# Kernel tuning notes

Hardware: AMD Instinct MI355X
Metric: run time of the kernel (lower is better)

## Reference

```python
import jax, jax.numpy as jnp
import numpy as np
import math

B, S, E, H, L, C, DFF = 8, 1024, 512, 8, 2, 8921, 2048
DH = E // H
LN_EPS = 1e-5


def _make_pe(max_len, d):
    pos = np.arange(max_len, dtype=np.float32)[:, None]
    div = np.exp(np.arange(0, d, 2, dtype=np.float32) * (-math.log(10000.0) / d))
    pe = np.zeros((max_len, d), dtype=np.float32)
    pe[:, 0::2] = np.sin(pos * div)
    pe[:, 1::2] = np.cos(pos * div)
    return jnp.asarray(pe)


def setup_inputs() -> dict:
    key = jax.random.key(0)
    ks = jax.random.split(key, 16)
    sc = 0.02
    return {
        'inputs': jax.random.normal(ks[0], (B, S, E), jnp.float32),
        'pe': _make_pe(S, E),
        'label_mat': jax.random.normal(ks[1], (C, E), jnp.float32) * sc,
        'l1_w': jax.random.normal(ks[2], (E, E), jnp.float32) * sc,
        'l1_b': jnp.zeros((E,), jnp.float32),
        'fc_w': jax.random.normal(ks[3], (C, E), jnp.float32) * sc,
        'fc_b': jnp.zeros((C,), jnp.float32),
        'in_proj_w': jax.random.normal(ks[4], (L, 3 * E, E), jnp.float32) * sc,
        'in_proj_b': jnp.zeros((L, 3 * E), jnp.float32),
        'out_proj_w': jax.random.normal(ks[5], (L, E, E), jnp.float32) * sc,
        'out_proj_b': jnp.zeros((L, E), jnp.float32),
        'ln1_w': jnp.ones((L, E), jnp.float32),
        'ln1_b': jnp.zeros((L, E), jnp.float32),
        'ln2_w': jnp.ones((L, E), jnp.float32),
        'ln2_b': jnp.zeros((L, E), jnp.float32),
        'lin1_w': jax.random.normal(ks[6], (L, DFF, E), jnp.float32) * sc,
        'lin1_b': jnp.zeros((L, DFF), jnp.float32),
        'lin2_w': jax.random.normal(ks[7], (L, E, DFF), jnp.float32) * sc,
        'lin2_b': jnp.zeros((L, E), jnp.float32),
    }


def _ln(x, g, b):
    mu = jnp.mean(x, axis=-1, keepdims=True)
    v = jnp.mean(jnp.square(x - mu), axis=-1, keepdims=True)
    return (x - mu) * jax.lax.rsqrt(v + LN_EPS) * g + b


def _encoder_layer(x, wqkv, bqkv, wo, bo, g1, b1, g2, b2, w1, bb1, w2, bb2):
    # x: [B,S,E]; post-norm torch TransformerEncoderLayer with relu
    qkv = x @ wqkv.T + bqkv                      # [B,S,3E]
    q, k, v = jnp.split(qkv, 3, axis=-1)
    q = q.reshape(B, S, H, DH)
    k = k.reshape(B, S, H, DH)
    v = v.reshape(B, S, H, DH)
    scores = jnp.einsum('bqhd,bkhd->bhqk', q, k) / math.sqrt(DH)
    attn = jax.nn.softmax(scores, axis=-1)
    o = jnp.einsum('bhqk,bkhd->bqhd', attn, v).reshape(B, S, E)
    o = o @ wo.T + bo
    x = _ln(x + o, g1, b1)
    ff = jax.nn.relu(x @ w1.T + bb1) @ w2.T + bb2
    return _ln(x + ff, g2, b2)


def reference(inputs, pe, label_mat, l1_w, l1_b, fc_w, fc_b,
              in_proj_w, in_proj_b, out_proj_w, out_proj_b,
              ln1_w, ln1_b, ln2_w, ln2_b,
              lin1_w, lin1_b, lin2_w, lin2_b):
    # faithful to source: pe is indexed by batch position (source bug)
    x = inputs * math.sqrt(E) + pe[:B][:, None, :]      # [B,S,E]
    for i in range(L):
        x = _encoder_layer(x, in_proj_w[i], in_proj_b[i], out_proj_w[i], out_proj_b[i],
                           ln1_w[i], ln1_b[i], ln2_w[i], ln2_b[i],
                           lin1_w[i], lin1_b[i], lin2_w[i], lin2_b[i])
    # label attention
    o1 = jnp.tanh(x @ l1_w.T + l1_b)                    # [B,S,E]
    scores = o1 @ label_mat.T                           # [B,S,C]
    attn_weights = jax.nn.softmax(scores, axis=1)       # over seq dim
    attn_weights = jnp.swapaxes(attn_weights, 1, 2)     # [B,C,S]
    weighted = attn_weights @ x                         # [B,C,E]
    # fused per-class linears: C tiny GEMVs -> one einsum
    outputs = jnp.einsum('bce,ce->bc', weighted, fc_w) + fc_b  # [B,C]
    return outputs, attn_weights
```

## Files before the change

kernel.cpp:

```cpp
#include <hip/hip_runtime.h>
#include <math.h>

#define BB   8
#define SS   1024
#define EE   512
#define HH   8
#define DHH  64
#define LLY  2
#define CC   8921
#define CP   9088
#define DFF_ 2048

typedef short          bf16x8 __attribute__((ext_vector_type(8)));
typedef float          f32x4  __attribute__((ext_vector_type(4)));
typedef unsigned short u16x4  __attribute__((ext_vector_type(4)));
typedef unsigned short u16x8  __attribute__((ext_vector_type(8)));

__device__ __forceinline__ float bf2f(unsigned short u) {
    return __uint_as_float(((unsigned int)u) << 16);
}
__device__ __forceinline__ unsigned short f2bf(float f) {
    unsigned int u = __float_as_uint(f);
    u = (u + 0x7FFFu + ((u >> 16) & 1u)) >> 16;
    return (unsigned short)u;
}
__device__ __forceinline__ void gload16(const void* g, void* l) {
    __builtin_amdgcn_global_load_lds(
        (const __attribute__((address_space(1))) void*)g,
        (__attribute__((address_space(3))) void*)l, 16, 0, 0);
}

__global__ __launch_bounds__(256) void cvt_bf16(const float* __restrict__ in,
                                                unsigned short* __restrict__ out,
                                                long n_in, long n_out)
{
    const long i4 = ((long)blockIdx.x * 256 + threadIdx.x) * 4;
    if (i4 >= n_out) return;
    u16x4 r;
    if (i4 < n_in) {
        const float4 v = *(const float4*)(in + i4);
        r[0] = f2bf(v.x); r[1] = f2bf(v.y); r[2] = f2bf(v.z); r[3] = f2bf(v.w);
    } else {
        r[0] = r[1] = r[2] = r[3] = 0;
    }
    *(u16x4*)(out + i4) = r;
}

__global__ __launch_bounds__(256) void embed_kernel(const float* __restrict__ in,
                                                    const float* __restrict__ pe,
                                                    float* __restrict__ x,
                                                    unsigned short* __restrict__ xb)
{
    const long i  = (long)blockIdx.x * 256 + threadIdx.x;
    const int  e4 = (int)(i & 127);
    const int  b  = (int)(i >> 17);
    float4 v = ((const float4*)in)[i];
    const float4 p = ((const float4*)pe)[b * 128 + e4];
    const float sc = 22.627416997969522f;
    v.x = v.x * sc + p.x;  v.y = v.y * sc + p.y;
    v.z = v.z * sc + p.z;  v.w = v.w * sc + p.w;
    ((float4*)x)[i] = v;
    u16x4 h; h[0] = f2bf(v.x); h[1] = f2bf(v.y); h[2] = f2bf(v.z); h[3] = f2bf(v.w);
    ((u16x4*)xb)[i] = h;
}

template<int FN>
__global__ __launch_bounds__(256) void gemm_mfma_t(const unsigned short* __restrict__ A,
                                                   const unsigned short* __restrict__ B,
                                                   const float* __restrict__ bias,
                                                   float* __restrict__ Cf,
                                                   unsigned short* __restrict__ Ch,
                                                   int M, int N, int K, int Mlim,
                                                   long sAz, long sBz, long sCz,
                                                   int act, int mode)
{
    __shared__ unsigned short As[128 * 64];
    __shared__ unsigned short Bs[32 * FN * 64];
    const int t  = threadIdx.x;
    const int wv = t >> 6, ln = t & 63;
    const int wr = wv >> 1, wc = wv & 1;
    const int lr = ln & 15, lg = ln >> 4;
    const int m0 = blockIdx.x * 128, n0 = blockIdx.y * (32 * FN);
    const int z  = blockIdx.z;
    const unsigned short* Ab = A + (long)z * sAz;
    const unsigned short* Bb = B + (long)z * sBz;

    const int srow = ln >> 3;
    const int ucol = ((ln & 7) ^ srow) << 3;

    f32x4 acc[4][FN];
    #pragma unroll
    for (int i = 0; i < 4; ++i)
        #pragma unroll
        for (int j = 0; j < FN; ++j)
            acc[i][j] = (f32x4){0.f, 0.f, 0.f, 0.f};

    int rA[4], rB[FN];
    #pragma unroll
    for (int f = 0; f < 4; ++f) rA[f] = wr * 64 + f * 16 + lr;
    #pragma unroll
    for (int f = 0; f < FN; ++f) rB[f] = wc * (16 * FN) + f * 16 + lr;

    for (int k0 = 0; k0 < K; k0 += 64) {
        __syncthreads();
        #pragma unroll
        for (int c = 0; c < 4; ++c) {
            const int q   = (wv << 2) + c;
            const int row = (q << 3) + srow;
            gload16(Ab + (long)(m0 + row) * K + k0 + ucol, (char*)As + (q << 10));
        }
        #pragma unroll
        for (int c = 0; c < FN; ++c) {
            const int q   = wv * FN + c;
            const int row = (q << 3) + srow;
            gload16(Bb + (long)(n0 + row) * K + k0 + ucol, (char*)Bs + (q << 10));
        }
        __syncthreads();
        #pragma unroll
        for (int kk = 0; kk < 2; ++kk) {
            bf16x8 af[4], bg[FN];
            const int s = (kk << 2) + lg;
            #pragma unroll
            for (int f = 0; f < 4; ++f)
                af[f] = *(const bf16x8*)((const char*)As + rA[f] * 128 + ((s ^ (rA[f] & 7)) << 4));
            #pragma unroll
            for (int f = 0; f < FN; ++f)
                bg[f] = *(const bf16x8*)((const char*)Bs + rB[f] * 128 + ((s ^ (rB[f] & 7)) << 4));
            #pragma unroll
            for (int i = 0; i < 4; ++i)
                #pragma unroll
                for (int j = 0; j < FN; ++j)
                    acc[i][j] = __builtin_amdgcn_mfma_f32_16x16x32_bf16(af[i], bg[j], acc[i][j], 0, 0, 0);
        }
    }

    const long zC = (long)z * sCz;
    #pragma unroll
    for (int fm = 0; fm < 4; ++fm) {
        #pragma unroll
        for (int reg = 0; reg < 4; ++reg) {
            const int gm = m0 + wr * 64 + fm * 16 + lg * 4 + reg;
            if (gm >= Mlim) continue;
            #pragma unroll
            for (int fn = 0; fn < FN; ++fn) {
                const int gn = n0 + wc * (16 * FN) + fn * 16 + lr;
                float v = acc[fm][fn][reg];
                if (bias) v += bias[gn];
                if (act == 1)      v = fmaxf(v, 0.f);
                else if (act == 2) v = tanhf(v);
                if (mode & 1) Cf[zC + (long)gm * N + gn] = v;
                if (mode & 2) Ch[zC + (long)gm * N + gn] = f2bf(v);
            }
        }
    }
}

__device__ __forceinline__ void label_swizzle(int& bx, int& by, int& bz)
{
    const int flat = blockIdx.x + 71 * (blockIdx.y + 8 * blockIdx.z);
    const int swz  = (flat & 7) * 568 + (flat >> 3);
    bx = swz >> 6;
    by = swz & 7;
    bz = (swz >> 3) & 7;
}

template<bool BF16RAW>
__global__ __launch_bounds__(256) void gemm_scores_t(const unsigned short* __restrict__ A,
                                                     const unsigned short* __restrict__ B,
                                                     float* __restrict__ attnW,
                                                     unsigned short* __restrict__ rawb,
                                                     float2* __restrict__ stats)
{
    __shared__ unsigned short As[128 * 64];
    __shared__ unsigned short Bs[128 * 64];
    int bx, by, bz;
    label_swizzle(bx, by, bz);
    const int t  = threadIdx.x;
    const int wv = t >> 6, ln = t & 63;
    const int wr = wv >> 1, wc = wv & 1;
    const int lr = ln & 15, lg = ln >> 4;
    const int m0 = bx * 128, n0 = by * 128;
    const int z  = bz;
    const unsigned short* Bb = B + (long)z * SS * EE;

    const int srow = ln >> 3;
    const int ucol = ((ln & 7) ^ srow) << 3;

    f32x4 acc[4][4];
    #pragma unroll
    for (int i = 0; i < 4; ++i)
        #pragma unroll
        for (int j = 0; j < 4; ++j)
            acc[i][j] = (f32x4){0.f, 0.f, 0.f, 0.f};

    int rA[4], rB[4];
    #pragma unroll
    for (int f = 0; f < 4; ++f) {
        rA[f] = wr * 64 + f * 16 + lr;
        rB[f] = wc * 64 + f * 16 + lr;
    }

    for (int k0 = 0; k0 < EE; k0 += 64) {
        __syncthreads();
        #pragma unroll
        for (int c = 0; c < 4; ++c) {
            const int q   = (wv << 2) + c;
            const int row = (q << 3) + srow;
            gload16(A  + (long)(m0 + row) * EE + k0 + ucol, (char*)As + (q << 10));
            gload16(Bb + (long)(n0 + row) * EE + k0 + ucol, (char*)Bs + (q << 10));
        }
        __syncthreads();
        #pragma unroll
        for (int kk = 0; kk < 2; ++kk) {
            bf16x8 af[4], bg[4];
            const int s = (kk << 2) + lg;
            #pragma unroll
            for (int f = 0; f < 4; ++f) {
                af[f] = *(const bf16x8*)((const char*)As + rA[f] * 128 + ((s ^ (rA[f] & 7)) << 4));
                bg[f] = *(const bf16x8*)((const char*)Bs + rB[f] * 128 + ((s ^ (rB[f] & 7)) << 4));
            }
            #pragma unroll
            for (int i = 0; i < 4; ++i)
                #pragma unroll
                for (int j = 0; j < 4; ++j)
                    acc[i][j] = __builtin_amdgcn_mfma_f32_16x16x32_bf16(af[i], bg[j], acc[i][j], 0, 0, 0);
        }
    }

    float* aw = attnW + (long)z * CC * SS;
    unsigned short* rb = rawb + (long)z * CC * SS;
    #pragma unroll
    for (int fm = 0; fm < 4; ++fm) {
        #pragma unroll
        for (int reg = 0; reg < 4; ++reg) {
            const int r = m0 + wr * 64 + fm * 16 + lg * 4 + reg;
            const float v0 = acc[fm][0][reg], v1 = acc[fm][1][reg];
            const float v2 = acc[fm][2][reg], v3 = acc[fm][3][reg];
            if (r < CC) {
                #pragma unroll
                for (int fn = 0; fn < 4; ++fn) {
                    const int sn = n0 + wc * 64 + fn * 16 + lr;
                    if (BF16RAW) rb[(long)r * SS + sn] = f2bf(acc[fm][fn][reg]);
                    else         aw[(long)r * SS + sn] = acc[fm][fn][reg];
                }
            }
            float mx = fmaxf(fmaxf(v0, v1), fmaxf(v2, v3));
            mx = fmaxf(mx, __shfl_xor(mx, 1));
            mx = fmaxf(mx, __shfl_xor(mx, 2));
            mx = fmaxf(mx, __shfl_xor(mx, 4));
            mx = fmaxf(mx, __shfl_xor(mx, 8));
            float sm = __expf(v0 - mx) + __expf(v1 - mx) + __expf(v2 - mx) + __expf(v3 - mx);
            sm += __shfl_xor(sm, 1); sm += __shfl_xor(sm, 2);
            sm += __shfl_xor(sm, 4); sm += __shfl_xor(sm, 8);
            if (lr == 0 && r < CC)
                stats[((long)z * CP + r) * 16 + by * 2 + wc] = make_float2(mx, sm);
        }
    }
}

__global__ __launch_bounds__(256) void merge_stats(const float2* __restrict__ stats,
                                                   float2* __restrict__ rowstat)
{
    const long idx = (long)blockIdx.x * 256 + threadIdx.x;
    if (idx >= (long)BB * CP) return;
    const int c = (int)(idx % CP);
    if (c >= CC) return;
    const float2* s = stats + idx * 16;
    float mx = -1e30f;
    #pragma unroll
    for (int i = 0; i < 16; ++i) mx = fmaxf(mx, s[i].x);
    float tot = 0.f;
    #pragma unroll
    for (int i = 0; i < 16; ++i) tot += s[i].y * __expf(s[i].x - mx);
    rowstat[idx] = make_float2(mx, 1.f / tot);
}

template<bool BF16RAW>
__global__ __launch_bounds__(256) void gemm_label_final_t(const unsigned short* __restrict__ A,
                                                          const unsigned short* __restrict__ B,
                                                          float* __restrict__ attnW,
                                                          const unsigned short* __restrict__ rawb,
                                                          const float2* __restrict__ rowstat,
                                                          float* __restrict__ out)
{
    __shared__ unsigned short As[128 * 64];
    __shared__ unsigned short Bs[128 * 64];
    int bx, by, bz;
    label_swizzle(bx, by, bz);
    const int t  = threadIdx.x;
    const int wv = t >> 6, ln = t & 63;
    const int wr = wv >> 1, wc = wv & 1;
    const int lr = ln & 15, lg = ln >> 4;
    const int m0 = bx * 128, n0 = by * 128;
    const int z  = bz;
    const unsigned short* Bb = B + (long)z * SS * EE;

    const int srow = ln >> 3;
    const int ucol = ((ln & 7) ^ srow) << 3;

    f32x4 acc[4][4];
    #pragma unroll
    for (int i = 0; i < 4; ++i)
        #pragma unroll
        for (int j = 0; j < 4; ++j)
            acc[i][j] = (f32x4){0.f, 0.f, 0.f, 0.f};

    int rA[4], rB[4];
    #pragma unroll
    for (int f = 0; f < 4; ++f) {
        rA[f] = wr * 64 + f * 16 + lr;
        rB[f] = wc * 64 + f * 16 + lr;
    }

    for (int k0 = 0; k0 < EE; k0 += 64) {
        __syncthreads();
        #pragma unroll
        for (int c = 0; c < 4; ++c) {
            const int q   = (wv << 2) + c;
            const int row = (q << 3) + srow;
            gload16(A  + (long)(m0 + row) * EE + k0 + ucol, (char*)As + (q << 10));
            gload16(Bb + (long)(n0 + row) * EE + k0 + ucol, (char*)Bs + (q << 10));
        }
        __syncthreads();
        #pragma unroll
        for (int kk = 0; kk < 2; ++kk) {
            bf16x8 af[4], bg[4];
            const int s = (kk << 2) + lg;
            #pragma unroll
            for (int f = 0; f < 4; ++f) {
                af[f] = *(const bf16x8*)((const char*)As + rA[f] * 128 + ((s ^ (rA[f] & 7)) << 4));
                bg[f] = *(const bf16x8*)((const char*)Bs + rB[f] * 128 + ((s ^ (rB[f] & 7)) << 4));
            }
            #pragma unroll
            for (int i = 0; i < 4; ++i)
                #pragma unroll
                for (int j = 0; j < 4; ++j)
                    acc[i][j] = __builtin_amdgcn_mfma_f32_16x16x32_bf16(af[i], bg[j], acc[i][j], 0, 0, 0);
        }
    }

    float* aw = attnW + (long)z * CC * SS;
    const unsigned short* rb = rawb + (long)z * CC * SS;
    const float2* rs = rowstat + (long)z * CP;
    float* outb = out + (long)z * CC;
    #pragma unroll
    for (int fm = 0; fm < 4; ++fm) {
        #pragma unroll
        for (int reg = 0; reg < 4; ++reg) {
            const int r = m0 + wr * 64 + fm * 16 + lg * 4 + reg;
            float pacc = 0.f;
            if (r < CC) {
                const float2 st = rs[r];
                #pragma unroll
                for (int fn = 0; fn < 4; ++fn) {
                    const int sn = n0 + wc * 64 + fn * 16 + lr;
                    const float raw = BF16RAW ? bf2f(rb[(long)r * SS + sn])
                                              : aw[(long)r * SS + sn];
                    const float p = __expf(raw - st.x) * st.y;
                    aw[(long)r * SS + sn] = p;
                    pacc += p * acc[fm][fn][reg];
                }
            }
            pacc += __shfl_xor(pacc, 1);
            pacc += __shfl_xor(pacc, 2);
            pacc += __shfl_xor(pacc, 4);
            pacc += __shfl_xor(pacc, 8);
            if (lr == 0 && r < CC) atomicAdd(&outb[r], pacc);
        }
    }
}

__global__ __launch_bounds__(256) void vtrans(const unsigned short* __restrict__ qkv,
                                              unsigned short* __restrict__ Vt)
{
    __shared__ unsigned short tile[64][72];
    const int bh = blockIdx.y, b = bh >> 3, h = bh & 7;
    const int s0 = blockIdx.x << 6;
    const int t  = threadIdx.x;
    const int r  = t >> 3;
    const int c8 = (t & 7) << 3;
    const unsigned short* vb = qkv + (long)b * SS * 1536 + 2 * EE + h * DHH;
    #pragma unroll
    for (int rr = 0; rr < 64; rr += 32)
        *(u16x8*)&tile[r + rr][c8] = *(const u16x8*)(vb + (long)(s0 + r + rr) * 1536 + c8);
    __syncthreads();
    #pragma unroll
    for (int rr = 0; rr < 64; rr += 32) {
        const int d = r + rr;
        u16x8 o;
        #pragma unroll
        for (int j = 0; j < 8; ++j) o[j] = tile[c8 + j][d];
        *(u16x8*)(Vt + ((long)bh * DHH + d) * SS + s0 + c8) = o;
    }
}

__global__ __launch_bounds__(512) void flash_mfma(const unsigned short* __restrict__ qkv,
                                                  const unsigned short* __restrict__ Vt,
                                                  unsigned short* __restrict__ o)
{
    __shared__ unsigned short sK[64 * 64];
    __shared__ unsigned short sV[64 * 64];
    __shared__ unsigned short sP[8][16 * 64];
    const int t  = threadIdx.x;
    const int wv = t >> 6, ln = t & 63;
    const int lr = ln & 15, lg = ln >> 4;
    const int bh = blockIdx.y, b = bh >> 3, h = bh & 7;
    const int q0 = (blockIdx.x << 7) + (wv << 4);

    const unsigned short* qb = qkv + (long)b * SS * 1536 + h * DHH;
    const unsigned short* kb = qb + EE;
    const unsigned short* vt = Vt + (long)bh * DHH * SS;
    unsigned short* pw = sP[wv];

    const int srow = ln >> 3;
    const int ucol = ((ln & 7) ^ srow) << 3;

    bf16x8 aq[2];
    #pragma unroll
    for (int c = 0; c < 2; ++c)
        aq[c] = *(const bf16x8*)(qb + (long)(q0 + lr) * 1536 + (c << 5) + (lg << 3));

    float m_[4], l_[4];
    f32x4 accO[4];
    #pragma unroll
    for (int r = 0; r < 4; ++r) { m_[r] = -1e30f; l_[r] = 0.f; }
    #pragma unroll
    for (int n = 0; n < 4; ++n) accO[n] = (f32x4){0.f, 0.f, 0.f, 0.f};

    for (int s0 = 0; s0 < SS; s0 += 64) {
        __syncthreads();
        {
            const int row = (wv << 3) + srow;
            gload16(kb + (long)(s0 + row) * 1536 + ucol, (char*)sK + (wv << 10));
            gload16(vt + (long)row * SS + s0 + ucol,     (char*)sV + (wv << 10));
        }
        __syncthreads();

        f32x4 accS[4];
        #pragma unroll
        for (int sj = 0; sj < 4; ++sj) accS[sj] = (f32x4){0.f, 0.f, 0.f, 0.f};
        #pragma unroll
        for (int c = 0; c < 2; ++c) {
            const int slot = (c << 2) + lg;
            #pragma unroll
            for (int sj = 0; sj < 4; ++sj) {
                const int rw = (sj << 4) + lr;
                const bf16x8 kf = *(const bf16x8*)((const char*)sK + rw * 128 + ((slot ^ (rw & 7)) << 4));
                accS[sj] = __builtin_amdgcn_mfma_f32_16x16x32_bf16(aq[c], kf, accS[sj], 0, 0, 0);
            }
        }
        #pragma unroll
        for (int reg = 0; reg < 4; ++reg) {
            float sc0 = accS[0][reg] * 0.125f, sc1 = accS[1][reg] * 0.125f;
            float sc2 = accS[2][reg] * 0.125f, sc3 = accS[3][reg] * 0.125f;
            float mx = fmaxf(fmaxf(sc0, sc1), fmaxf(sc2, sc3));
            mx = fmaxf(mx, __shfl_xor(mx, 1));
            mx = fmaxf(mx, __shfl_xor(mx, 2));
            mx = fmaxf(mx, __shfl_xor(mx, 4));
            mx = fmaxf(mx, __shfl_xor(mx, 8));
            const float mnew = fmaxf(m_[reg], mx);
            const float f = __expf(m_[reg] - mnew);
            m_[reg] = mnew;
            sc0 = __expf(sc0 - mnew); sc1 = __expf(sc1 - mnew);
            sc2 = __expf(sc2 - mnew); sc3 = __expf(sc3 - mnew);
            accS[0][reg] = sc0; accS[1][reg] = sc1;
            accS[2][reg] = sc2; accS[3][reg] = sc3;
            float ss = sc0 + sc1 + sc2 + sc3;
            ss += __shfl_xor(ss, 1); ss += __shfl_xor(ss, 2);
            ss += __shfl_xor(ss, 4); ss += __shfl_xor(ss, 8);
            l_[reg] = l_[reg] * f + ss;
            #pragma unroll
            for (int n = 0; n < 4; ++n) accO[n][reg] *= f;
        }
        #pragma unroll
        for (int sj = 0; sj < 4; ++sj) {
            #pragma unroll
            for (int reg = 0; reg < 4; ++reg) {
                const int q = (lg << 2) + reg;
                const int s = (sj << 4) + lr;
                const int byte = (q << 7) + (((s >> 3) ^ (q & 7)) << 4) + ((s & 7) << 1);
                *(unsigned short*)((char*)pw + byte) = f2bf(accS[sj][reg]);
            }
        }
        #pragma unroll
        for (int c2 = 0; c2 < 2; ++c2) {
            const int pslot = ((c2 << 2) + lg) ^ (lr & 7);
            const bf16x8 pa = *(const bf16x8*)((const char*)pw + (lr << 7) + (pslot << 4));
            const int vslot = (c2 << 2) + lg;
            #pragma unroll
            for (int n = 0; n < 4; ++n) {
                const int rw = (n << 4) + lr;
                const bf16x8 vf = *(const bf16x8*)((const char*)sV + rw * 128 + ((vslot ^ (rw & 7)) << 4));
                accO[n] = __builtin_amdgcn_mfma_f32_16x16x32_bf16(pa, vf, accO[n], 0, 0, 0);
            }
        }
    }

    #pragma unroll
    for (int reg = 0; reg < 4; ++reg) {
        const float inv = 1.f / l_[reg];
        unsigned short* orow = o + (long)(b * SS + q0 + (lg << 2) + reg) * EE + h * DHH;
        #pragma unroll
        for (int n = 0; n < 4; ++n)
            orow[(n << 4) + lr] = f2bf(accO[n][reg] * inv);
    }
}

__global__ __launch_bounds__(256) void ln_fused(float* __restrict__ x,
                                                unsigned short* __restrict__ xb,
                                                const float* __restrict__ o,
                                                const float* __restrict__ g,
                                                const float* __restrict__ bta)
{
    const long row = blockIdx.x;
    float* xr = x + row * EE;
    unsigned short* hb = xb + row * EE;
    const float* orr = o + row * EE;
    const int t = threadIdx.x;
    const float v0 = xr[t] + orr[t];
    const float v1 = xr[t + 256] + orr[t + 256];
    float s = v0 + v1;
    #pragma unroll
    for (int off = 1; off < 64; off <<= 1) s += __shfl_xor(s, off);
    __shared__ float r1[4], r2[4];
    if ((t & 63) == 0) r1[t >> 6] = s;
    __syncthreads();
    const float mu = (r1[0] + r1[1] + r1[2] + r1[3]) * (1.f / EE);
    const float d0 = v0 - mu, d1 = v1 - mu;
    float q = d0 * d0 + d1 * d1;
    #pragma unroll
    for (int off = 1; off < 64; off <<= 1) q += __shfl_xor(q, off);
    if ((t & 63) == 0) r2[t >> 6] = q;
    __syncthreads();
    const float rs = rsqrtf((r2[0] + r2[1] + r2[2] + r2[3]) * (1.f / EE) + 1e-5f);
    const float y0 = d0 * rs * g[t]       + bta[t];
    const float y1 = d1 * rs * g[t + 256] + bta[t + 256];
    xr[t] = y0;  xr[t + 256] = y1;
    hb[t] = f2bf(y0);  hb[t + 256] = f2bf(y1);
}

__global__ __launch_bounds__(256) void init_out(float* __restrict__ out,
                                                const float* __restrict__ fcb)
{
    const int i = blockIdx.x * 256 + threadIdx.x;
    if (i < BB * CC) out[i] = fcb[i % CC];
}

extern "C" void kernel_launch(void* const* d_in, const int* in_sizes, int n_in,
                              void* d_out, int out_size, void* d_ws, size_t ws_size,
                              hipStream_t stream)
{
    const float* inp   = (const float*)d_in[0];
    const float* pe    = (const float*)d_in[1];
    const float* label = (const float*)d_in[2];
    const float* l1w   = (const float*)d_in[3];
    const float* l1b   = (const float*)d_in[4];
    const float* fcw   = (const float*)d_in[5];
    const float* fcb   = (const float*)d_in[6];
    const float* ipw   = (const float*)d_in[7];
    const float* ipb   = (const float*)d_in[8];
    const float* opw   = (const float*)d_in[9];
    const float* opb   = (const float*)d_in[10];
    const float* g1    = (const float*)d_in[11];
    const float* b1    = (const float*)d_in[12];
    const float* g2    = (const float*)d_in[13];
    const float* b2    = (const float*)d_in[14];
    const float* w1    = (const float*)d_in[15];
    const float* bb1   = (const float*)d_in[16];
    const float* w2    = (const float*)d_in[17];
    const float* bb2   = (const float*)d_in[18];

    char* wp = (char*)d_ws;
    float* x = (float*)wp;                 wp += (long)BB * SS * EE * 4;
    unsigned short* xb = (unsigned short*)wp;  wp += (long)BB * SS * EE * 2;
    float* bufo = (float*)wp;              wp += (long)BB * SS * EE * 4;
    unsigned short* big = (unsigned short*)wp; wp += (long)BB * SS * DFF_ * 2;
    unsigned short* ob  = (unsigned short*)wp; wp += (long)BB * SS * EE * 2;
    unsigned short* Vtb = (unsigned short*)wp; wp += (long)BB * HH * DHH * SS * 2;
    unsigned short* ipwb = (unsigned short*)wp; wp += (long)LLY * 3 * EE * EE * 2;
    unsigned short* opwb = (unsigned short*)wp; wp += (long)LLY * EE * EE * 2;
    unsigned short* w1b  = (unsigned short*)wp; wp += (long)LLY * DFF_ * EE * 2;
    unsigned short* w2b  = (unsigned short*)wp; wp += (long)LLY * EE * DFF_ * 2;
    unsigned short* l1wb = (unsigned short*)wp; wp += (long)EE * EE * 2;
    unsigned short* labelb = (unsigned short*)wp; wp += (long)CP * EE * 2;
    unsigned short* fcwb   = (unsigned short*)wp; wp += (long)CP * EE * 2;
    float2* stats   = (float2*)wp;         wp += (long)BB * CP * 16 * 8;
    float2* rowstat = (float2*)wp;         wp += (long)BB * CP * 8;
    unsigned short* rawb = (unsigned short*)wp;
    const long raw_bytes = (long)BB * CC * SS * 2;
    const bool bf16raw = ((long)ws_size >= (wp - (char*)d_ws) + raw_bytes);

    float* out0  = (float*)d_out;
    float* attnW = out0 + BB * CC;

    {
        const long n1 = (long)LLY * 3 * EE * EE;
        cvt_bf16<<<(int)((n1 / 4 + 255) / 256), 256, 0, stream>>>(ipw, ipwb, n1, n1);
        const long n2 = (long)LLY * EE * EE;
        cvt_bf16<<<(int)((n2 / 4 + 255) / 256), 256, 0, stream>>>(opw, opwb, n2, n2);
        const long n3 = (long)LLY * DFF_ * EE;
        cvt_bf16<<<(int)((n3 / 4 + 255) / 256), 256, 0, stream>>>(w1, w1b, n3, n3);
        cvt_bf16<<<(int)((n3 / 4 + 255) / 256), 256, 0, stream>>>(w2, w2b, n3, n3);
        const long n4 = (long)EE * EE;
        cvt_bf16<<<(int)((n4 / 4 + 255) / 256), 256, 0, stream>>>(l1w, l1wb, n4, n4);
        const long n5i = (long)CC * EE, n5o = (long)CP * EE;
        cvt_bf16<<<(int)((n5o / 4 + 255) / 256), 256, 0, stream>>>(label, labelb, n5i, n5o);
        cvt_bf16<<<(int)((n5o / 4 + 255) / 256), 256, 0, stream>>>(fcw, fcwb, n5i, n5o);
    }

    const int M = BB * SS;

    embed_kernel<<<4096, 256, 0, stream>>>(inp, pe, x, xb);

    for (int l = 0; l < LLY; ++l) {
        gemm_mfma_t<4><<<dim3(64, 12, 1), 256, 0, stream>>>(xb, ipwb + (long)l * 3 * EE * EE,
                                                            ipb + l * 3 * EE, nullptr, big,
                                                            M, 3 * EE, EE, M, 0, 0, 0, 0, 2);
        vtrans<<<dim3(16, 64), 256, 0, stream>>>(big, Vtb);
        flash_mfma<<<dim3(8, 64), 512, 0, stream>>>(big, Vtb, ob);
        gemm_mfma_t<2><<<dim3(64, 8, 1), 256, 0, stream>>>(ob, opwb + (long)l * EE * EE,
                                                           opb + l * EE, bufo, nullptr,
                                                           M, EE, EE, M, 0, 0, 0, 0, 1);
        ln_fused<<<M, 256, 0, stream>>>(x, xb, bufo, g1 + l * EE, b1 + l * EE);
        gemm_mfma_t<4><<<dim3(64, 16, 1), 256, 0, stream>>>(xb, w1b + (long)l * DFF_ * EE,
                                                            bb1 + l * DFF_, nullptr, big,
                                                            M, DFF_, EE, M, 0, 0, 0, 1, 2);
        gemm_mfma_t<2><<<dim3(64, 8, 1), 256, 0, stream>>>(big, w2b + (long)l * EE * DFF_,
                                                           bb2 + l * EE, bufo, nullptr,
                                                           M, EE, DFF_, M, 0, 0, 0, 0, 1);
        ln_fused<<<M, 256, 0, stream>>>(x, xb, bufo, g2 + l * EE, b2 + l * EE);
    }

    gemm_mfma_t<2><<<dim3(64, 8, 1), 256, 0, stream>>>(xb, l1wb, l1b, nullptr, ob,
                                                       M, EE, EE, M, 0, 0, 0, 2, 2);
    if (bf16raw)
        gemm_scores_t<true><<<dim3(CP / 128, SS / 128, BB), 256, 0, stream>>>(labelb, ob, attnW, rawb, stats);
    else
        gemm_scores_t<false><<<dim3(CP / 128, SS / 128, BB), 256, 0, stream>>>(labelb, ob, attnW, rawb, stats);
    merge_stats<<<(int)(((long)BB * CP + 255) / 256), 256, 0, stream>>>(stats, rowstat);
    init_out<<<(BB * CC + 255) / 256, 256, 0, stream>>>(out0, fcb);
    if (bf16raw)
        gemm_label_final_t<true><<<dim3(CP / 128, SS / 128, BB), 256, 0, stream>>>(fcwb, xb, attnW, rawb, rowstat, out0);
    else
        gemm_label_final_t<false><<<dim3(CP / 128, SS / 128, BB), 256, 0, stream>>>(fcwb, xb, attnW, rawb, rowstat, out0);
}
```

Measured before the change: 1.012 ms.

## Loop over sequence tiles inside label-final GEMM to cut atomics

The final label GEMM kernel now launches one block per (class tile, batch) and loops over all eight sequence tiles internally. Per-row partial sums accumulate in registers, so each class row gets one atomicAdd instead of eight. The cost is 8x fewer blocks (568 instead of 4544), which lowers parallelism and latency hiding on a large GPU, and the block swizzle is replaced with a simple custom mapping.

```diff
diff --git a/kernel.cpp b/kernel.cpp
--- a/kernel.cpp
+++ b/kernel.cpp
@@ -275,6 +275,13 @@
     rowstat[idx] = make_float2(mx, 1.f / tot);
 }
 
+__global__ __launch_bounds__(256) void init_out(float* __restrict__ out,
+                                                const float* __restrict__ fcb)
+{
+    const int i = blockIdx.x * 256 + threadIdx.x;
+    if (i < BB * CC) out[i] = fcb[i % CC];
+}
+
 template<bool BF16RAW>
 __global__ __launch_bounds__(256) void gemm_label_final_t(const unsigned short* __restrict__ A,
                                                           const unsigned short* __restrict__ B,
@@ -285,25 +292,19 @@
 {
     __shared__ unsigned short As[128 * 64];
     __shared__ unsigned short Bs[128 * 64];
-    int bx, by, bz;
-    label_swizzle(bx, by, bz);
+    const int flat = blockIdx.x + 71 * blockIdx.z;
+    const int swz  = (flat & 7) * 71 + (flat >> 3);
+    const int bx   = swz >> 3;
+    const int z    = swz & 7;
     const int t  = threadIdx.x;
     const int wv = t >> 6, ln = t & 63;
     const int wr = wv >> 1, wc = wv & 1;
     const int lr = ln & 15, lg = ln >> 4;
-    const int m0 = bx * 128, n0 = by * 128;
-    const int z  = bz;
+    const int m0 = bx * 128;
     const unsigned short* Bb = B + (long)z * SS * EE;
 
     const int srow = ln >> 3;
     const int ucol = ((ln & 7) ^ srow) << 3;
-
-    f32x4 acc[4][4];
-    #pragma unroll
-    for (int i = 0; i < 4; ++i)
-        #pragma unroll
-        for (int j = 0; j < 4; ++j)
-            acc[i][j] = (f32x4){0.f, 0.f, 0.f, 0.f};
 
     int rA[4], rB[4];
     #pragma unroll
@@ -312,55 +313,81 @@
         rB[f] = wc * 64 + f * 16 + lr;
     }
 
-    for (int k0 = 0; k0 < EE; k0 += 64) {
-        __syncthreads();
-        #pragma unroll
-        for (int c = 0; c < 4; ++c) {
-            const int q   = (wv << 2) + c;
-            const int row = (q << 3) + srow;
-            gload16(A  + (long)(m0 + row) * EE + k0 + ucol, (char*)As + (q << 10));
-            gload16(Bb + (long)(n0 + row) * EE + k0 + ucol, (char*)Bs + (q << 10));
-        }
-        __syncthreads();
-        #pragma unroll
-        for (int kk = 0; kk < 2; ++kk) {
-            bf16x8 af[4], bg[4];
-            const int s = (kk << 2) + lg;
-            #pragma unroll
-            for (int f = 0; f < 4; ++f) {
-                af[f] = *(const bf16x8*)((const char*)As + rA[f] * 128 + ((s ^ (rA[f] & 7)) << 4));
-                bg[f] = *(const bf16x8*)((const char*)Bs + rB[f] * 128 + ((s ^ (rB[f] & 7)) << 4));
-            }
-            #pragma unroll
-            for (int i = 0; i < 4; ++i)
-                #pragma unroll
-                for (int j = 0; j < 4; ++j)
-                    acc[i][j] = __builtin_amdgcn_mfma_f32_16x16x32_bf16(af[i], bg[j], acc[i][j], 0, 0, 0);
-        }
-    }
-
     float* aw = attnW + (long)z * CC * SS;
     const unsigned short* rb = rawb + (long)z * CC * SS;
     const float2* rs = rowstat + (long)z * CP;
+
+    float outAcc[4][4];
+    #pragma unroll
+    for (int i = 0; i < 4; ++i)
+        #pragma unroll
+        for (int j = 0; j < 4; ++j)
+            outAcc[i][j] = 0.f;
+
+    for (int sy = 0; sy < 8; ++sy) {
+        const int n0 = sy << 7;
+        f32x4 acc[4][4];
+        #pragma unroll
+        for (int i = 0; i < 4; ++i)
+            #pragma unroll
+            for (int j = 0; j < 4; ++j)
+                acc[i][j] = (f32x4){0.f, 0.f, 0.f, 0.f};
+
+        for (int k0 = 0; k0 < EE; k0 += 64) {
+            __syncthreads();
+            #pragma unroll
+            for (int c = 0; c < 4; ++c) {
+                const int q   = (wv << 2) + c;
+                const int row = (q << 3) + srow;
+                gload16(A  + (long)(m0 + row) * EE + k0 + ucol, (char*)As + (q << 10));
+                gload16(Bb + (long)(n0 + row) * EE + k0 + ucol, (char*)Bs + (q << 10));
+            }
+            __syncthreads();
+            #pragma unroll
+            for (int kk = 0; kk < 2; ++kk) {
+                bf16x8 af[4], bg[4];
+                const int s = (kk << 2) + lg;
+                #pragma unroll
+                for (int f = 0; f < 4; ++f) {
+                    af[f] = *(const bf16x8*)((const char*)As + rA[f] * 128 + ((s ^ (rA[f] & 7)) << 4));
+                    bg[f] = *(const bf16x8*)((const char*)Bs + rB[f] * 128 + ((s ^ (rB[f] & 7)) << 4));
+                }
+                #pragma unroll
+                for (int i = 0; i < 4; ++i)
+                    #pragma unroll
+                    for (int j = 0; j < 4; ++j)
+                        acc[i][j] = __builtin_amdgcn_mfma_f32_16x16x32_bf16(af[i], bg[j], acc[i][j], 0, 0, 0);
+            }
+        }
+
+        #pragma unroll
+        for (int fm = 0; fm < 4; ++fm) {
+            #pragma unroll
+            for (int reg = 0; reg < 4; ++reg) {
+                const int r = m0 + wr * 64 + fm * 16 + lg * 4 + reg;
+                if (r < CC) {
+                    const float2 st = rs[r];
+                    #pragma unroll
+                    for (int fn = 0; fn < 4; ++fn) {
+                        const int sn = n0 + wc * 64 + fn * 16 + lr;
+                        const float raw = BF16RAW ? bf2f(rb[(long)r * SS + sn])
+                                                  : aw[(long)r * SS + sn];
+                        const float p = __expf(raw - st.x) * st.y;
+                        aw[(long)r * SS + sn] = p;
+                        outAcc[fm][reg] += p * acc[fm][fn][reg];
+                    }
+                }
+            }
+        }
+    }
+
     float* outb = out + (long)z * CC;
     #pragma unroll
     for (int fm = 0; fm < 4; ++fm) {
         #pragma unroll
         for (int reg = 0; reg < 4; ++reg) {
             const int r = m0 + wr * 64 + fm * 16 + lg * 4 + reg;
-            float pacc = 0.f;
-            if (r < CC) {
-                const float2 st = rs[r];
-                #pragma unroll
-                for (int fn = 0; fn < 4; ++fn) {
-                    const int sn = n0 + wc * 64 + fn * 16 + lr;
-                    const float raw = BF16RAW ? bf2f(rb[(long)r * SS + sn])
-                                              : aw[(long)r * SS + sn];
-                    const float p = __expf(raw - st.x) * st.y;
-                    aw[(long)r * SS + sn] = p;
-                    pacc += p * acc[fm][fn][reg];
-                }
-            }
+            float pacc = outAcc[fm][reg];
             pacc += __shfl_xor(pacc, 1);
             pacc += __shfl_xor(pacc, 2);
             pacc += __shfl_xor(pacc, 4);
@@ -539,13 +566,6 @@
     hb[t] = f2bf(y0);  hb[t + 256] = f2bf(y1);
 }
 
-__global__ __launch_bounds__(256) void init_out(float* __restrict__ out,
-                                                const float* __restrict__ fcb)
-{
-    const int i = blockIdx.x * 256 + threadIdx.x;
-    if (i < BB * CC) out[i] = fcb[i % CC];
-}
-
 extern "C" void kernel_launch(void* const* d_in, const int* in_sizes, int n_in,
                               void* d_out, int out_size, void* d_ws, size_t ws_size,
                               hipStream_t stream)
@@ -640,7 +660,7 @@
     merge_stats<<<(int)(((long)BB * CP + 255) / 256), 256, 0, stream>>>(stats, rowstat);
     init_out<<<(BB * CC + 255) / 256, 256, 0, stream>>>(out0, fcb);
     if (bf16raw)
-        gemm_label_final_t<true><<<dim3(CP / 128, SS / 128, BB), 256, 0, stream>>>(fcwb, xb, attnW, rawb, rowstat, out0);
+        gemm_label_final_t<true><<<dim3(71, 1, 8), 256, 0, stream>>>(fcwb, xb, attnW, rawb, rowstat, out0);
     else
-        gemm_label_final_t<false><<<dim3(CP / 128, SS / 128, BB), 256, 0, stream>>>(fcwb, xb, attnW, rawb, rowstat, out0);
-}
+        gemm_label_final_t<false><<<dim3(71, 1, 8), 256, 0, stream>>>(fcwb, xb, attnW, rawb, rowstat, out0);
+}
```

Result: slower. 1.261 ms (+24.5%).
